# Kernel optimization log

Measured on AMD Instinct MI355X. Metric: run time of the kernel, lower is better.

Reference implementation:

```python
import jax, jax.numpy as jnp
import numpy as np

DIM, A, B_FAC, BATCH = 256, 8, 8, 2048
IN_F, OUT_F = A * DIM, B_FAC * DIM  # 2048, 2048


def _make_masks():
    ri = np.arange(IN_F) // A       # input block index per row
    cj = np.arange(OUT_F) // B_FAC  # output block index per col
    diag = ri[:, None] == cj[None, :]
    off = ri[:, None] < cj[None, :]
    return diag, off

DIAG_NP, OFF_NP = _make_masks()
DIAG_M = jnp.asarray(DIAG_NP)
OFF_M = jnp.asarray(OFF_NP)


def setup_inputs() -> dict:
    key = jax.random.key(0)
    k1, k2, k3, k4 = jax.random.split(key, 4)
    x = jax.random.normal(k1, (BATCH, IN_F), dtype=jnp.float32)
    accum_blocks = jax.random.normal(k2, (BATCH, DIM, A, A), dtype=jnp.float32)
    # parameter init mirrors the torch module
    w = jax.random.normal(k3, (IN_F, OUT_F), dtype=jnp.float32) / np.sqrt(IN_F + OUT_F)
    weight = jnp.where(DIAG_M, jnp.log(jnp.abs(w)), w)
    log_diag = jnp.log(jax.random.uniform(k4, (1, OUT_F), dtype=jnp.float32,
                                          minval=0.01, maxval=1.0))
    bias = jnp.zeros((1, OUT_F), dtype=jnp.float32)
    return {"x": x, "accum_blocks": accum_blocks, "weight": weight,
            "log_diag": log_diag, "bias": bias}


def log_dot_exp(lx, ly):
    # result[...,i,j] = logsumexp_k(lx[...,i,k] + ly[...,k,j]); stable via max-shift + GEMM
    mx = jnp.max(lx, axis=-1, keepdims=True)   # [B,D,i,1]
    my = jnp.max(ly, axis=-2, keepdims=True)   # [B,D,1,j]
    s = jnp.einsum('bdik,bdkj->bdij', jnp.exp(lx - mx), jnp.exp(ly - my))
    return jnp.log(s) + mx + my


def reference(x, accum_blocks, weight, log_diag, bias):
    # masked weight construction: exp on the block diagonal, raw off-diagonal, 0 elsewhere
    w = jnp.where(DIAG_M, jnp.exp(weight), jnp.where(OFF_M, weight, 0.0))
    w_norm = jnp.sqrt(jnp.sum(w * w, axis=-1, keepdims=True))  # [IN_F,1], L2 over output dim
    w_eff = jnp.exp(log_diag) * (w / w_norm)
    # log of the diagonal blocks of the effective weight
    ldb_full = log_diag + weight - jnp.log(w_norm)             # [IN_F, OUT_F]
    ldb = ldb_full[DIAG_NP].reshape(1, DIM, A, B_FAC)          # static bool mask -> static gather
    y = x @ w_eff + bias                                       # [B, OUT_F]
    ldb_b = jnp.broadcast_to(ldb, (x.shape[0], DIM, A, B_FAC))
    accum = log_dot_exp(accum_blocks, ldb_b)                   # [B, DIM, A, B_FAC]
    return y, accum
```

## Files before the change

kernel.cpp:

```cpp
#include <hip/hip_runtime.h>
#include <math.h>

#define IN_F 2048
#define OUT_F 2048
#define BATCH 2048

typedef float4 f4;
typedef __attribute__((ext_vector_type(4))) float f32x4;
typedef __attribute__((ext_vector_type(8))) short bf16x8;
typedef __attribute__((ext_vector_type(4))) short bf16x4;

__device__ inline unsigned short f2bh(float f) {
    unsigned u = __float_as_uint(f);
    u += 0x7FFF + ((u >> 16) & 1);
    return (unsigned short)(u >> 16);
}
__device__ inline float bh2f(unsigned short h) {
    return __uint_as_float(((unsigned)h) << 16);
}


__global__ __launch_bounds__(256) void prep_rows_k(const float* __restrict__ weight,
                                                   const float* __restrict__ log_diag,
                                                   float* __restrict__ invnorm,
                                                   float* __restrict__ ldb) {
    const int i  = blockIdx.x;
    const int ri = i >> 3;
    const int t  = threadIdx.x;
    const f4* wrow = reinterpret_cast<const f4*>(weight + (size_t)i * OUT_F);
    f4 v0 = wrow[t * 2];
    f4 v1 = wrow[t * 2 + 1];
    float raw[8] = {v0.x, v0.y, v0.z, v0.w, v1.x, v1.y, v1.z, v1.w};

    float ss = 0.0f;
    if (t == ri) {
        #pragma unroll
        for (int e = 0; e < 8; ++e) { float m = expf(raw[e]); ss += m * m; }
    } else if (t > ri) {
        #pragma unroll
        for (int e = 0; e < 8; ++e) ss += raw[e] * raw[e];
    }
    #pragma unroll
    for (int o = 32; o > 0; o >>= 1) ss += __shfl_xor(ss, o, 64);
    __shared__ float part[4];
    if ((t & 63) == 0) part[t >> 6] = ss;
    __syncthreads();
    float total = part[0] + part[1] + part[2] + part[3];
    float norm  = sqrtf(total);

    if (t == 0) invnorm[i] = 1.0f / norm;
    if (t == ri) {
        float logn = logf(norm);
        int a = i & 7;
        #pragma unroll
        for (int b = 0; b < 8; ++b)
            ldb[ri * 64 + a * 8 + b] = log_diag[ri * 8 + b] + raw[b] - logn;
    }
}

__global__ __launch_bounds__(256) void prep_ldb_k(const float* __restrict__ ldb,
                                                  const float* __restrict__ log_diag,
                                                  float* __restrict__ myv,
                                                  float* __restrict__ eY,
                                                  float* __restrict__ expld) {
    int t = blockIdx.x * 256 + threadIdx.x;
    expld[t] = expf(log_diag[t]);
    int d = t >> 3, j = t & 7;
    float m = -INFINITY;
    #pragma unroll
    for (int k = 0; k < 8; ++k) m = fmaxf(m, ldb[d * 64 + k * 8 + j]);
    myv[t] = m;
    #pragma unroll
    for (int k = 0; k < 8; ++k) eY[d * 64 + k * 8 + j] = expf(ldb[d * 64 + k * 8 + j] - m);
}

#define BK 32
#define TILE_BYTES 24576

__device__ inline int swz(int row, int kc) {
    int R = row >> 2;
    int c = ((row & 3) << 2) | kc;
    return (R << 8) | (((c ^ (R & 15)) & 15) << 4);
}

__global__ __launch_bounds__(256, 3) void gemm_mfma_k(const float* __restrict__ x,
                                                      const float* __restrict__ weight,
                                                      const float* __restrict__ invnorm,
                                                      const float* __restrict__ expld,
                                                      const float* __restrict__ bias,
                                                      float* __restrict__ y) {
    __shared__ char lds[2 * TILE_BYTES];

    const int b  = blockIdx.x;
    const int q  = (b & 7) | (((b >> 8) & 1) << 3);
    const int it = (b >> 3) & 31;
    const int m0 = it * 64;
    const int jL = q * 64;
    const int jR = (31 - q) * 64;
    const int KL = jL + 64;
    const int KR = jR + 64;
    const int nt  = KR >> 5;
    const int ntL = KL >> 5;

    const int tid = threadIdx.x;
    const int l   = tid & 63;
    const int w   = tid >> 6;
    const int wr  = w >> 1, wc = w & 1;
    const int l15 = l & 15, h = (l >> 4) & 3;

    int mA[2], koA[2], wbA[2];
    #pragma unroll
    for (int i = 0; i < 2; ++i) {
        int fi = tid + (i << 8);
        mA[i] = fi >> 3;
        int c8 = fi & 7;
        koA[i] = c8 << 2;
        wbA[i] = swz(mA[i], c8 >> 1) + ((c8 & 1) << 3);
    }
    const int sB  = tid >> 7;
    const int tt  = tid & 127;
    const int nB  = tt & 63;
    const int kh  = tt >> 6;
    const int ngB = (sB ? jR : jL) + nB;
    const int cjB = ngB >> 3;
    const int rB  = (sB << 6) + nB;
    const int wbB0 = swz(rB, kh << 1);
    const int wbB1 = swz(rB, (kh << 1) | 1);

    int raA[2], raB[4];
    #pragma unroll
    for (int mi = 0; mi < 2; ++mi) raA[mi] = swz(32 * wr + 16 * mi + l15, h);
    #pragma unroll
    for (int nj = 0; nj < 4; ++nj) {
        int rb = ((nj >> 1) << 6) + 32 * wc + ((nj & 1) << 4);
        raB[nj] = swz(rb + l15, h);
    }

    f32x4 acc[2][4];
    #pragma unroll
    for (int mi = 0; mi < 2; ++mi)
        #pragma unroll
        for (int nj = 0; nj < 4; ++nj) acc[mi][nj] = (f32x4)0.0f;

    f4 rxa[2], riva[2];
    float rw[16];

    auto LOAD = [&](int k0) {
        #pragma unroll
        for (int i = 0; i < 2; ++i) {
            rxa[i]  = *reinterpret_cast<const f4*>(x + (size_t)(m0 + mA[i]) * IN_F + k0 + koA[i]);
            riva[i] = *reinterpret_cast<const f4*>(invnorm + k0 + koA[i]);
        }
        if (sB || (k0 < KL)) {
            #pragma unroll
            for (int i = 0; i < 16; ++i)
                rw[i] = weight[(size_t)(k0 + (kh << 4) + i) * OUT_F + ngB];
        }
    };

    auto COMMIT = [&](int k0, int buf) {
        char* base = lds + buf * TILE_BYTES;
        #pragma unroll
        for (int i = 0; i < 2; ++i) {
            bf16x4 h4, l4;
            const float* xp = reinterpret_cast<const float*>(&rxa[i]);
            const float* ip = reinterpret_cast<const float*>(&riva[i]);
            #pragma unroll
            for (int c = 0; c < 4; ++c) {
                float xs = xp[c] * ip[c];
                unsigned short hb = f2bh(xs);
                h4[c] = (short)hb;
                l4[c] = (short)f2bh(xs - bh2f(hb));
            }
            *reinterpret_cast<bf16x4*>(base + wbA[i]) = h4;
            *reinterpret_cast<bf16x4*>(base + 4096 + wbA[i]) = l4;
        }
        if (sB || (k0 < KL)) {
            bf16x8 h8a, l8a, h8b, l8b;
            #pragma unroll
            for (int i = 0; i < 16; ++i) {
                int k  = k0 + (kh << 4) + i;
                int rk = k >> 3;
                float v = (cjB < rk) ? 0.0f : ((cjB == rk) ? __expf(rw[i]) : rw[i]);
                unsigned short hb = f2bh(v);
                unsigned short lb = f2bh(v - bh2f(hb));
                if (i < 8) { h8a[i] = (short)hb; l8a[i] = (short)lb; }
                else       { h8b[i - 8] = (short)hb; l8b[i - 8] = (short)lb; }
            }
            *reinterpret_cast<bf16x8*>(base + 8192  + wbB0) = h8a;
            *reinterpret_cast<bf16x8*>(base + 8192  + wbB1) = h8b;
            *reinterpret_cast<bf16x8*>(base + 16384 + wbB0) = l8a;
            *reinterpret_cast<bf16x8*>(base + 16384 + wbB1) = l8b;
        }
    };

    LOAD(0);
    COMMIT(0, 0);
    if (nt > 1) LOAD(BK);
    __syncthreads();

    for (int t = 0; t < nt; ++t) {
        const int cur = t & 1;
        if (t + 1 < nt) COMMIT((t + 1) << 5, cur ^ 1);
        if (t + 2 < nt) LOAD((t + 2) << 5);
        {
            const char* base = lds + cur * TILE_BYTES;
            const bool full = (t < ntL);
            bf16x8 ah[2], al[2], bh[4], bl[4];
            #pragma unroll
            for (int mi = 0; mi < 2; ++mi) {
                ah[mi] = *reinterpret_cast<const bf16x8*>(base + raA[mi]);
                al[mi] = *reinterpret_cast<const bf16x8*>(base + 4096 + raA[mi]);
            }
            #pragma unroll
            for (int nj = 0; nj < 4; ++nj) {
                if (nj >= 2 || full) {
                    bh[nj] = *reinterpret_cast<const bf16x8*>(base + 8192  + raB[nj]);
                    bl[nj] = *reinterpret_cast<const bf16x8*>(base + 16384 + raB[nj]);
                }
            }
            #pragma unroll
            for (int mi = 0; mi < 2; ++mi)
                #pragma unroll
                for (int nj = 0; nj < 4; ++nj) {
                    if (nj >= 2 || full) {
                        acc[mi][nj] = __builtin_amdgcn_mfma_f32_16x16x32_bf16(ah[mi], bh[nj], acc[mi][nj], 0, 0, 0);
                        acc[mi][nj] = __builtin_amdgcn_mfma_f32_16x16x32_bf16(al[mi], bh[nj], acc[mi][nj], 0, 0, 0);
                        acc[mi][nj] = __builtin_amdgcn_mfma_f32_16x16x32_bf16(ah[mi], bl[nj], acc[mi][nj], 0, 0, 0);
                    }
                }
        }
        __syncthreads();
    }

    #pragma unroll
    for (int mi = 0; mi < 2; ++mi)
        #pragma unroll
        for (int nj = 0; nj < 4; ++nj) {
            int nb  = ((nj >> 1) ? jR : jL) + 32 * wc + ((nj & 1) << 4);
            int col = nb + l15;
            float el = expld[col];
            float bs = bias[col];
            #pragma unroll
            for (int j = 0; j < 4; ++j) {
                int row = m0 + 32 * wr + 16 * mi + ((l >> 4) << 2) + j;
                y[(size_t)row * OUT_F + col] = ((const float*)&acc[mi][nj])[j] * el + bs;
            }
        }
}

__global__ __launch_bounds__(256) void accum_k(const float* __restrict__ ab,
                                               const float* __restrict__ eY,
                                               const float* __restrict__ myv,
                                               float* __restrict__ out) {
    __shared__ float lsE[32 * 68];
    __shared__ float lsM[256];

    const int blk = blockIdx.x;
    const int t   = threadIdx.x;
    const int d0  = (blk * 32) & 255;

    #pragma unroll
    for (int hh = 0; hh < 2; ++hh) {
        int idx4 = t + hh * 256;
        int lin  = idx4 * 4;
        int dd = lin >> 6, c = lin & 63;
        f4 v = *reinterpret_cast<const f4*>(eY + d0 * 64 + lin);
        *reinterpret_cast<f4*>(&lsE[dd * 68 + c]) = v;
    }
    lsM[t] = myv[d0 * 8 + t];
    __syncthreads();

    const size_t r = (size_t)blk * 256 + t;
    const f4* lxp = reinterpret_cast<const f4*>(ab + r * 8);
    f4 l0 = lxp[0], l1 = lxp[1];
    float lx[8] = {l0.x, l0.y, l0.z, l0.w, l1.x, l1.y, l1.z, l1.w};

    float mx = lx[0];
    #pragma unroll
    for (int k = 1; k < 8; ++k) mx = fmaxf(mx, lx[k]);
    float el[8];
    #pragma unroll
    for (int k = 0; k < 8; ++k) el[k] = __expf(lx[k] - mx);

    const int dd = t >> 3;
    float o[8];
    #pragma unroll
    for (int j = 0; j < 8; ++j) {
        float s = 0.0f;
        #pragma unroll
        for (int k = 0; k < 8; ++k)
            s = fmaf(el[k], lsE[dd * 68 + k * 8 + j], s);
        o[j] = __logf(s) + mx + lsM[dd * 8 + j];
    }
    f4 o0 = {o[0], o[1], o[2], o[3]};
    f4 o1 = {o[4], o[5], o[6], o[7]};
    f4* op = reinterpret_cast<f4*>(out + r * 8);
    op[0] = o0; op[1] = o1;
}

extern "C" void kernel_launch(void* const* d_in, const int* in_sizes, int n_in,
                              void* d_out, int out_size, void* d_ws, size_t ws_size,
                              hipStream_t stream) {
    const float* x        = (const float*)d_in[0];
    const float* ab       = (const float*)d_in[1];
    const float* weight   = (const float*)d_in[2];
    const float* log_diag = (const float*)d_in[3];
    const float* bias     = (const float*)d_in[4];

    float* y     = (float*)d_out;
    float* accum = (float*)d_out + (size_t)BATCH * OUT_F;

    float* ws      = (float*)d_ws;
    float* invnorm = ws;
    float* ldb     = ws + 2048;
    float* expld   = ws + 18432;
    float* myv     = ws + 20480;
    float* eY      = ws + 22528;

    hipLaunchKernelGGL(prep_rows_k, dim3(2048), dim3(256), 0, stream,
                       weight, log_diag, invnorm, ldb);
    hipLaunchKernelGGL(prep_ldb_k, dim3(8), dim3(256), 0, stream,
                       ldb, log_diag, myv, eY, expld);
    hipLaunchKernelGGL(gemm_mfma_k, dim3(512), dim3(256), 0, stream,
                       x, weight, invnorm, expld, bias, y);
    hipLaunchKernelGGL(accum_k, dim3(16384), dim3(256), 0, stream,
                       ab, eY, myv, accum);
}
```

Measured before the change: 352.9 us.

## Pre-split operands to bf16 hi/lo tiles and stream them into LDS directly

Adds two conversion kernels that turn x and the masked, normalised, scaled weight into pre-swizzled bf16 hi/lo tiles, stored in the accum output buffer as scratch. The GEMM then fills LDS with global_load_lds DMA instead of loading through registers and converting inside the main loop, and folds invnorm and exp(log_diag) into the weight. This removes per-tile conversion ALU work and register staging from the GEMM. The cost is two extra launches and a round trip of about 32MB through memory. The accum kernel also switches to vectorised LDS reads.

```diff
diff --git a/kernel.cpp b/kernel.cpp
--- a/kernel.cpp
+++ b/kernel.cpp
@@ -8,15 +8,20 @@
 typedef float4 f4;
 typedef __attribute__((ext_vector_type(4))) float f32x4;
 typedef __attribute__((ext_vector_type(8))) short bf16x8;
-typedef __attribute__((ext_vector_type(4))) short bf16x4;
-
-__device__ inline unsigned short f2bh(float f) {
+
+__device__ __forceinline__ unsigned short f2bh(float f) {
     unsigned u = __float_as_uint(f);
     u += 0x7FFF + ((u >> 16) & 1);
     return (unsigned short)(u >> 16);
 }
-__device__ inline float bh2f(unsigned short h) {
+__device__ __forceinline__ float bh2f(unsigned short h) {
     return __uint_as_float(((unsigned)h) << 16);
+}
+
+__device__ __forceinline__ void gload16(const char* g, char* l) {
+    __builtin_amdgcn_global_load_lds(
+        (const __attribute__((address_space(1))) unsigned int*)g,
+        (__attribute__((address_space(3))) unsigned int*)l, 16, 0, 0);
 }
 
 
@@ -74,177 +79,189 @@
     for (int k = 0; k < 8; ++k) eY[d * 64 + k * 8 + j] = expf(ldb[d * 64 + k * 8 + j] - m);
 }
 
-#define BK 32
-#define TILE_BYTES 24576
-
-__device__ inline int swz(int row, int kc) {
-    int R = row >> 2;
-    int c = ((row & 3) << 2) | kc;
-    return (R << 8) | (((c ^ (R & 15)) & 15) << 4);
-}
-
-__global__ __launch_bounds__(256, 3) void gemm_mfma_k(const float* __restrict__ x,
-                                                      const float* __restrict__ weight,
-                                                      const float* __restrict__ invnorm,
-                                                      const float* __restrict__ expld,
-                                                      const float* __restrict__ bias,
-                                                      float* __restrict__ y) {
-    __shared__ char lds[2 * TILE_BYTES];
+__global__ __launch_bounds__(256) void conv_x_k(const float* __restrict__ x,
+                                                char* __restrict__ scratch) {
+    const int gid = blockIdx.x * 256 + threadIdx.x;
+    const int c  = gid & 3;
+    const int r  = (gid >> 2) & 63;
+    const int kt = (gid >> 8) & 63;
+    const int mt = gid >> 14;
+    const int h  = (c ^ (r >> 1)) & 3;
+    const int m  = mt * 64 + r;
+    const int k  = kt * 32 + h * 8;
+    const f4* xp = reinterpret_cast<const f4*>(x + (size_t)m * IN_F + k);
+    f4 a = xp[0], b = xp[1];
+    float v[8] = {a.x, a.y, a.z, a.w, b.x, b.y, b.z, b.w};
+    bf16x8 h8, l8;
+    #pragma unroll
+    for (int i = 0; i < 8; ++i) {
+        unsigned short hb = f2bh(v[i]);
+        h8[i] = (short)hb;
+        l8[i] = (short)f2bh(v[i] - bh2f(hb));
+    }
+    *reinterpret_cast<bf16x8*>(scratch + (size_t)gid * 16) = h8;
+    *reinterpret_cast<bf16x8*>(scratch + (8u << 20) + (size_t)gid * 16) = l8;
+}
+
+__global__ __launch_bounds__(256) void conv_w_k(const float* __restrict__ weight,
+                                                const float* __restrict__ invnorm,
+                                                const float* __restrict__ expld,
+                                                char* __restrict__ scratch) {
+    const int blk = blockIdx.x;
+    const int ct  = blk >> 6;
+    const int kt  = blk & 63;
+    if (kt >= 2 * ct + 2) return;
+
+    __shared__ unsigned short sh_hi[32 * 64], sh_lo[32 * 64];
+    const int t  = threadIdx.x;
+    const int kr = t >> 3;
+    const int ns = (t & 7) * 8;
+    const int k  = kt * 32 + kr;
+    const int n0 = ct * 64 + ns;
+    const int rk = k >> 3;
+
+    const f4* wp = reinterpret_cast<const f4*>(weight + (size_t)k * OUT_F + n0);
+    f4 a = wp[0], b = wp[1];
+    f4 e0 = *reinterpret_cast<const f4*>(expld + n0);
+    f4 e1 = *reinterpret_cast<const f4*>(expld + n0 + 4);
+    const float inv = invnorm[k];
+    float vv[8] = {a.x, a.y, a.z, a.w, b.x, b.y, b.z, b.w};
+    float ee[8] = {e0.x, e0.y, e0.z, e0.w, e1.x, e1.y, e1.z, e1.w};
+    #pragma unroll
+    for (int i = 0; i < 8; ++i) {
+        int cj = (n0 + i) >> 3;
+        float v = (cj < rk) ? 0.0f : ((cj == rk) ? __expf(vv[i]) : vv[i]);
+        v *= inv * ee[i];
+        unsigned short hb = f2bh(v);
+        sh_hi[kr * 64 + ns + i] = hb;
+        sh_lo[kr * 64 + ns + i] = f2bh(v - bh2f(hb));
+    }
+    __syncthreads();
+
+    const int r = t >> 2, c = t & 3;
+    const int h = (c ^ (r >> 1)) & 3;
+    bf16x8 oh, ol;
+    #pragma unroll
+    for (int i = 0; i < 8; ++i) {
+        oh[i] = (short)sh_hi[(h * 8 + i) * 64 + r];
+        ol[i] = (short)sh_lo[(h * 8 + i) * 64 + r];
+    }
+    const size_t tb = (size_t)(ct * 64 + kt) * 4096 + (size_t)t * 16;
+    *reinterpret_cast<bf16x8*>(scratch + (16u << 20) + tb) = oh;
+    *reinterpret_cast<bf16x8*>(scratch + (24u << 20) + tb) = ol;
+}
+
+#define LDS_STEP 24576
+__global__ __launch_bounds__(256, 2) void gemm_mfma2_k(const char* __restrict__ scratch,
+                                                       const float* __restrict__ bias,
+                                                       float* __restrict__ y) {
+    __shared__ __align__(16) char lds[2 * LDS_STEP];
 
     const int b  = blockIdx.x;
     const int q  = (b & 7) | (((b >> 8) & 1) << 3);
-    const int it = (b >> 3) & 31;
-    const int m0 = it * 64;
-    const int jL = q * 64;
-    const int jR = (31 - q) * 64;
-    const int KL = jL + 64;
-    const int KR = jR + 64;
-    const int nt  = KR >> 5;
-    const int ntL = KL >> 5;
+    const int mt = (b >> 3) & 31;
+    const int m0 = mt * 64;
+    const int jL = q * 64, jR = (31 - q) * 64;
+    const int ctL = q, ctR = 31 - q;
+    const int ntL = 2 * (q + 1), nt = 2 * (32 - q);
 
     const int tid = threadIdx.x;
     const int l   = tid & 63;
     const int w   = tid >> 6;
     const int wr  = w >> 1, wc = w & 1;
-    const int l15 = l & 15, h = (l >> 4) & 3;
-
-    int mA[2], koA[2], wbA[2];
-    #pragma unroll
-    for (int i = 0; i < 2; ++i) {
-        int fi = tid + (i << 8);
-        mA[i] = fi >> 3;
-        int c8 = fi & 7;
-        koA[i] = c8 << 2;
-        wbA[i] = swz(mA[i], c8 >> 1) + ((c8 & 1) << 3);
-    }
-    const int sB  = tid >> 7;
-    const int tt  = tid & 127;
-    const int nB  = tt & 63;
-    const int kh  = tt >> 6;
-    const int ngB = (sB ? jR : jL) + nB;
-    const int cjB = ngB >> 3;
-    const int rB  = (sB << 6) + nB;
-    const int wbB0 = swz(rB, kh << 1);
-    const int wbB1 = swz(rB, (kh << 1) | 1);
-
-    int raA[2], raB[4];
-    #pragma unroll
-    for (int mi = 0; mi < 2; ++mi) raA[mi] = swz(32 * wr + 16 * mi + l15, h);
-    #pragma unroll
-    for (int nj = 0; nj < 4; ++nj) {
-        int rb = ((nj >> 1) << 6) + 32 * wc + ((nj & 1) << 4);
-        raB[nj] = swz(rb + l15, h);
+    const int l15 = l & 15, h = l >> 4;
+
+    const char* aHi = scratch;
+    const char* aLo = scratch + (8u  << 20);
+    const char* bHi = scratch + (16u << 20);
+    const char* bLo = scratch + (24u << 20);
+
+    int raA[2], raB[2];
+    #pragma unroll
+    for (int mi = 0; mi < 2; ++mi) {
+        int row = wr * 32 + mi * 16 + l15;
+        raA[mi] = row * 64 + (((h ^ (row >> 1)) & 3) << 4);
+    }
+    #pragma unroll
+    for (int nj = 0; nj < 2; ++nj) {
+        int row = wc * 32 + nj * 16 + l15;
+        raB[nj] = row * 64 + (((h ^ (row >> 1)) & 3) << 4);
     }
 
     f32x4 acc[2][4];
     #pragma unroll
     for (int mi = 0; mi < 2; ++mi)
         #pragma unroll
-        for (int nj = 0; nj < 4; ++nj) acc[mi][nj] = (f32x4)0.0f;
-
-    f4 rxa[2], riva[2];
-    float rw[16];
-
-    auto LOAD = [&](int k0) {
-        #pragma unroll
-        for (int i = 0; i < 2; ++i) {
-            rxa[i]  = *reinterpret_cast<const f4*>(x + (size_t)(m0 + mA[i]) * IN_F + k0 + koA[i]);
-            riva[i] = *reinterpret_cast<const f4*>(invnorm + k0 + koA[i]);
-        }
-        if (sB || (k0 < KL)) {
+        for (int cc = 0; cc < 4; ++cc) acc[mi][cc] = (f32x4)0.0f;
+
+    const int lane16 = tid << 4;
+    const int wbase  = (tid >> 6) << 10;
+
+    auto STAGE = [&](int buf, int ti) {
+        char* lb = lds + buf * LDS_STEP + wbase;
+        const size_t at = (size_t)(mt * 64 + ti) * 4096 + lane16;
+        gload16(aHi + at, lb);
+        gload16(aLo + at, lb + 4096);
+        const size_t btR = (size_t)(ctR * 64 + ti) * 4096 + lane16;
+        gload16(bHi + btR, lb + 12288);
+        gload16(bLo + btR, lb + 20480);
+        if (ti < ntL) {
+            const size_t btL = (size_t)(ctL * 64 + ti) * 4096 + lane16;
+            gload16(bHi + btL, lb + 8192);
+            gload16(bLo + btL, lb + 16384);
+        }
+    };
+
+    STAGE(0, 0);
+    __syncthreads();
+
+    int cur = 0;
+    for (int ti = 0; ti < nt; ++ti) {
+        if (ti + 1 < nt) STAGE(cur ^ 1, ti + 1);
+        const char* base = lds + cur * LDS_STEP;
+        const bool full = (ti < ntL);
+        bf16x8 ah[2], al[2], bh[4], bl[4];
+        #pragma unroll
+        for (int mi = 0; mi < 2; ++mi) {
+            ah[mi] = *reinterpret_cast<const bf16x8*>(base + raA[mi]);
+            al[mi] = *reinterpret_cast<const bf16x8*>(base + 4096 + raA[mi]);
+        }
+        #pragma unroll
+        for (int nj = 0; nj < 2; ++nj) {
+            bh[2 + nj] = *reinterpret_cast<const bf16x8*>(base + 12288 + raB[nj]);
+            bl[2 + nj] = *reinterpret_cast<const bf16x8*>(base + 20480 + raB[nj]);
+        }
+        if (full) {
             #pragma unroll
-            for (int i = 0; i < 16; ++i)
-                rw[i] = weight[(size_t)(k0 + (kh << 4) + i) * OUT_F + ngB];
-        }
-    };
-
-    auto COMMIT = [&](int k0, int buf) {
-        char* base = lds + buf * TILE_BYTES;
-        #pragma unroll
-        for (int i = 0; i < 2; ++i) {
-            bf16x4 h4, l4;
-            const float* xp = reinterpret_cast<const float*>(&rxa[i]);
-            const float* ip = reinterpret_cast<const float*>(&riva[i]);
+            for (int nj = 0; nj < 2; ++nj) {
+                bh[nj] = *reinterpret_cast<const bf16x8*>(base + 8192  + raB[nj]);
+                bl[nj] = *reinterpret_cast<const bf16x8*>(base + 16384 + raB[nj]);
+            }
+        }
+        #pragma unroll
+        for (int mi = 0; mi < 2; ++mi)
             #pragma unroll
-            for (int c = 0; c < 4; ++c) {
-                float xs = xp[c] * ip[c];
-                unsigned short hb = f2bh(xs);
-                h4[c] = (short)hb;
-                l4[c] = (short)f2bh(xs - bh2f(hb));
-            }
-            *reinterpret_cast<bf16x4*>(base + wbA[i]) = h4;
-            *reinterpret_cast<bf16x4*>(base + 4096 + wbA[i]) = l4;
-        }
-        if (sB || (k0 < KL)) {
-            bf16x8 h8a, l8a, h8b, l8b;
-            #pragma unroll
-            for (int i = 0; i < 16; ++i) {
-                int k  = k0 + (kh << 4) + i;
-                int rk = k >> 3;
-                float v = (cjB < rk) ? 0.0f : ((cjB == rk) ? __expf(rw[i]) : rw[i]);
-                unsigned short hb = f2bh(v);
-                unsigned short lb = f2bh(v - bh2f(hb));
-                if (i < 8) { h8a[i] = (short)hb; l8a[i] = (short)lb; }
-                else       { h8b[i - 8] = (short)hb; l8b[i - 8] = (short)lb; }
-            }
-            *reinterpret_cast<bf16x8*>(base + 8192  + wbB0) = h8a;
-            *reinterpret_cast<bf16x8*>(base + 8192  + wbB1) = h8b;
-            *reinterpret_cast<bf16x8*>(base + 16384 + wbB0) = l8a;
-            *reinterpret_cast<bf16x8*>(base + 16384 + wbB1) = l8b;
-        }
-    };
-
-    LOAD(0);
-    COMMIT(0, 0);
-    if (nt > 1) LOAD(BK);
-    __syncthreads();
-
-    for (int t = 0; t < nt; ++t) {
-        const int cur = t & 1;
-        if (t + 1 < nt) COMMIT((t + 1) << 5, cur ^ 1);
-        if (t + 2 < nt) LOAD((t + 2) << 5);
-        {
-            const char* base = lds + cur * TILE_BYTES;
-            const bool full = (t < ntL);
-            bf16x8 ah[2], al[2], bh[4], bl[4];
-            #pragma unroll
-            for (int mi = 0; mi < 2; ++mi) {
-                ah[mi] = *reinterpret_cast<const bf16x8*>(base + raA[mi]);
-                al[mi] = *reinterpret_cast<const bf16x8*>(base + 4096 + raA[mi]);
-            }
-            #pragma unroll
-            for (int nj = 0; nj < 4; ++nj) {
-                if (nj >= 2 || full) {
-                    bh[nj] = *reinterpret_cast<const bf16x8*>(base + 8192  + raB[nj]);
-                    bl[nj] = *reinterpret_cast<const bf16x8*>(base + 16384 + raB[nj]);
+            for (int cc = 0; cc < 4; ++cc) {
+                if (cc >= 2 || full) {
+                    acc[mi][cc] = __builtin_amdgcn_mfma_f32_16x16x32_bf16(ah[mi], bh[cc], acc[mi][cc], 0, 0, 0);
+                    acc[mi][cc] = __builtin_amdgcn_mfma_f32_16x16x32_bf16(al[mi], bh[cc], acc[mi][cc], 0, 0, 0);
+                    acc[mi][cc] = __builtin_amdgcn_mfma_f32_16x16x32_bf16(ah[mi], bl[cc], acc[mi][cc], 0, 0, 0);
                 }
             }
-            #pragma unroll
-            for (int mi = 0; mi < 2; ++mi)
-                #pragma unroll
-                for (int nj = 0; nj < 4; ++nj) {
-                    if (nj >= 2 || full) {
-                        acc[mi][nj] = __builtin_amdgcn_mfma_f32_16x16x32_bf16(ah[mi], bh[nj], acc[mi][nj], 0, 0, 0);
-                        acc[mi][nj] = __builtin_amdgcn_mfma_f32_16x16x32_bf16(al[mi], bh[nj], acc[mi][nj], 0, 0, 0);
-                        acc[mi][nj] = __builtin_amdgcn_mfma_f32_16x16x32_bf16(ah[mi], bl[nj], acc[mi][nj], 0, 0, 0);
-                    }
-                }
-        }
         __syncthreads();
+        cur ^= 1;
     }
 
     #pragma unroll
     for (int mi = 0; mi < 2; ++mi)
         #pragma unroll
-        for (int nj = 0; nj < 4; ++nj) {
-            int nb  = ((nj >> 1) ? jR : jL) + 32 * wc + ((nj & 1) << 4);
-            int col = nb + l15;
-            float el = expld[col];
+        for (int cc = 0; cc < 4; ++cc) {
+            int col = ((cc < 2) ? jL : jR) + wc * 32 + ((cc & 1) << 4) + l15;
             float bs = bias[col];
             #pragma unroll
             for (int j = 0; j < 4; ++j) {
-                int row = m0 + 32 * wr + 16 * mi + ((l >> 4) << 2) + j;
-                y[(size_t)row * OUT_F + col] = ((const float*)&acc[mi][nj])[j] * el + bs;
+                int row = m0 + wr * 32 + mi * 16 + (h << 2) + j;
+                y[(size_t)row * OUT_F + col] = ((const float*)&acc[mi][cc])[j] + bs;
             }
         }
 }
@@ -284,17 +301,24 @@
     for (int k = 0; k < 8; ++k) el[k] = __expf(lx[k] - mx);
 
     const int dd = t >> 3;
-    float o[8];
-    #pragma unroll
-    for (int j = 0; j < 8; ++j) {
-        float s = 0.0f;
-        #pragma unroll
-        for (int k = 0; k < 8; ++k)
-            s = fmaf(el[k], lsE[dd * 68 + k * 8 + j], s);
-        o[j] = __logf(s) + mx + lsM[dd * 8 + j];
-    }
-    f4 o0 = {o[0], o[1], o[2], o[3]};
-    f4 o1 = {o[4], o[5], o[6], o[7]};
+    float s[8] = {0, 0, 0, 0, 0, 0, 0, 0};
+    #pragma unroll
+    for (int k = 0; k < 8; ++k) {
+        float e = el[k];
+        f4 r0 = *reinterpret_cast<const f4*>(&lsE[dd * 68 + k * 8]);
+        f4 r1 = *reinterpret_cast<const f4*>(&lsE[dd * 68 + k * 8 + 4]);
+        s[0] = fmaf(e, r0.x, s[0]); s[1] = fmaf(e, r0.y, s[1]);
+        s[2] = fmaf(e, r0.z, s[2]); s[3] = fmaf(e, r0.w, s[3]);
+        s[4] = fmaf(e, r1.x, s[4]); s[5] = fmaf(e, r1.y, s[5]);
+        s[6] = fmaf(e, r1.z, s[6]); s[7] = fmaf(e, r1.w, s[7]);
+    }
+    f4 m0v = *reinterpret_cast<const f4*>(&lsM[dd * 8]);
+    f4 m1v = *reinterpret_cast<const f4*>(&lsM[dd * 8 + 4]);
+    f4 o0, o1;
+    o0.x = __logf(s[0]) + mx + m0v.x; o0.y = __logf(s[1]) + mx + m0v.y;
+    o0.z = __logf(s[2]) + mx + m0v.z; o0.w = __logf(s[3]) + mx + m0v.w;
+    o1.x = __logf(s[4]) + mx + m1v.x; o1.y = __logf(s[5]) + mx + m1v.y;
+    o1.z = __logf(s[6]) + mx + m1v.z; o1.w = __logf(s[7]) + mx + m1v.w;
     f4* op = reinterpret_cast<f4*>(out + r * 8);
     op[0] = o0; op[1] = o1;
 }
@@ -310,6 +334,7 @@
 
     float* y     = (float*)d_out;
     float* accum = (float*)d_out + (size_t)BATCH * OUT_F;
+    char*  scratch = (char*)accum;
 
     float* ws      = (float*)d_ws;
     float* invnorm = ws;
@@ -322,8 +347,11 @@
                        weight, log_diag, invnorm, ldb);
     hipLaunchKernelGGL(prep_ldb_k, dim3(8), dim3(256), 0, stream,
                        ldb, log_diag, myv, eY, expld);
-    hipLaunchKernelGGL(gemm_mfma_k, dim3(512), dim3(256), 0, stream,
-                       x, weight, invnorm, expld, bias, y);
+    hipLaunchKernelGGL(conv_x_k, dim3(2048), dim3(256), 0, stream, x, scratch);
+    hipLaunchKernelGGL(conv_w_k, dim3(2048), dim3(256), 0, stream,
+                       weight, invnorm, expld, scratch);
+    hipLaunchKernelGGL(gemm_mfma2_k, dim3(512), dim3(256), 0, stream,
+                       scratch, bias, y);
     hipLaunchKernelGGL(accum_k, dim3(16384), dim3(256), 0, stream,
                        ab, eY, myv, accum);
 }
```

Result: faster. 316.5 us (-10.3%).
